# Optimization experiments

Hardware: AMD Instinct MI355X
Metric: run time of the kernel (lower is better)

The kernel has to match this reference:

```python
import jax, jax.numpy as jnp
import numpy as np

B, H, W, D = 16, 14, 14, 512   # map_dim D == attention_dim A (required by broadcast add)
L, HID, A = 32, 512, 512


def setup_inputs() -> dict:
    key = jax.random.key(0)
    ks = jax.random.split(key, 8)
    s = 0.02
    return {
        "maps": jax.random.normal(ks[0], (B, H, W, D), jnp.float32),
        "hiddens": jax.random.normal(ks[1], (B, L, HID), jnp.float32),
        "W_hidden": jax.random.normal(ks[2], (A, HID), jnp.float32) * s,
        "b_hidden": jnp.zeros((A,), jnp.float32),
        "W_rect": jax.random.normal(ks[3], (1, A), jnp.float32) * s,
        "b_rect": jnp.zeros((1,), jnp.float32),
        "W_co": jax.random.normal(ks[4], (HID, D), jnp.float32) * s,
        "b_co": jnp.zeros((HID,), jnp.float32),
    }


def reference(maps, hiddens, W_hidden, b_hidden, W_rect, b_rect, W_co, b_co):
    b, h, w, d = maps.shape
    fmaps = maps.reshape(b, h * w, d)                       # (B, P, D)
    hlin = hiddens @ W_hidden.T + b_hidden                  # (B, L, A)
    # additive co-attention score: ReLU(fmaps + hlin) -> linear to scalar
    rect = jax.nn.relu(fmaps[:, None, :, :] + hlin[:, :, None, :])  # (B, L, P, A)
    scores = jnp.einsum('blpa,a->blp', rect, W_rect[0]) + b_rect[0]  # (B, L, P)
    attn = jax.nn.softmax(scores, axis=2)                   # softmax over pixels P
    ctx = jnp.einsum('blp,bpd->bld', attn, fmaps)           # (B, L, D)
    co_att = (ctx @ W_co.T + b_co) * hiddens                # (B, L, HID)
    return co_att, attn
```

## Files before the change

### kernel.cpp

```cpp
#include <hip/hip_runtime.h>
#include <math.h>

#define Bn   16
#define Ln   32
#define Pn   196
#define BLn  512

typedef __attribute__((ext_vector_type(8))) short short8;
typedef __attribute__((ext_vector_type(4))) float f32x4;

__device__ __forceinline__ unsigned f2bf_u(float x) {
    union { float f; unsigned u; } c; c.f = x;
    return (c.u + 0x7FFFu + ((c.u >> 16) & 1u)) >> 16;
}
__device__ __forceinline__ unsigned short f2bf(float x) { return (unsigned short)f2bf_u(x); }
__device__ __forceinline__ unsigned pack2(float lo, float hi) {
    return f2bf_u(lo) | (f2bf_u(hi) << 16);
}
__device__ __forceinline__ uint4 pack8(const float4 a, const float4 b) {
    uint4 r;
    r.x = pack2(a.x, a.y); r.y = pack2(a.z, a.w);
    r.z = pack2(b.x, b.y); r.w = pack2(b.z, b.w);
    return r;
}

template<int MODE>
__global__ __launch_bounds__(64) void mfma_gemm(
    const float* __restrict__ Af, const unsigned short* __restrict__ Ab,
    const float* __restrict__ B, const float* __restrict__ bias,
    const float* __restrict__ hmul, float* __restrict__ C)
{
    const int m0 = blockIdx.x * 32, n0 = blockIdx.y * 32;
    const int lane = threadIdx.x;
    __shared__ uint4 As[2048];
    __shared__ uint4 Bs[2048];

    const int quad = lane >> 4, mp = lane & 15;
    #pragma unroll 4
    for (int i = 0; i < 32; ++i) {
        const int t = i & 1, s = i >> 1;
        const int row  = t * 16 + mp;
        const int col8 = s * 4 + quad;
        uint4 av;
        if (MODE == 0) {
            const float* ap = Af + (size_t)(m0 + row) * 512 + col8 * 8;
            av = pack8(*(const float4*)ap, *(const float4*)(ap + 4));
        } else {
            av = *(const uint4*)(Ab + (size_t)(m0 + row) * 512 + col8 * 8);
        }
        const float* bp = B + (size_t)(n0 + row) * 512 + col8 * 8;
        As[i * 64 + lane] = av;
        Bs[i * 64 + lane] = pack8(*(const float4*)bp, *(const float4*)(bp + 4));
    }
    __syncthreads();

    f32x4 acc00 = {0.f,0.f,0.f,0.f};
    f32x4 acc01 = acc00, acc10 = acc00, acc11 = acc00;
    #pragma unroll
    for (int s = 0; s < 16; ++s) {
        const short8 a0 = *reinterpret_cast<const short8*>(&As[(2*s+0)*64 + lane]);
        const short8 a1 = *reinterpret_cast<const short8*>(&As[(2*s+1)*64 + lane]);
        const short8 b0 = *reinterpret_cast<const short8*>(&Bs[(2*s+0)*64 + lane]);
        const short8 b1 = *reinterpret_cast<const short8*>(&Bs[(2*s+1)*64 + lane]);
        acc00 = __builtin_amdgcn_mfma_f32_16x16x32_bf16(a0, b0, acc00, 0, 0, 0);
        acc01 = __builtin_amdgcn_mfma_f32_16x16x32_bf16(a0, b1, acc01, 0, 0, 0);
        acc10 = __builtin_amdgcn_mfma_f32_16x16x32_bf16(a1, b0, acc10, 0, 0, 0);
        acc11 = __builtin_amdgcn_mfma_f32_16x16x32_bf16(a1, b1, acc11, 0, 0, 0);
    }

    const int row4 = quad * 4, col = mp;
    const f32x4 accs[2][2] = { {acc00, acc01}, {acc10, acc11} };
    #pragma unroll
    for (int tm = 0; tm < 2; ++tm)
        #pragma unroll
        for (int tn = 0; tn < 2; ++tn)
            #pragma unroll
            for (int r = 0; r < 4; ++r) {
                const int m = m0 + tm*16 + row4 + r, n = n0 + tn*16 + col;
                float v = accs[tm][tn][r] + bias[n];
                if (MODE == 1) v *= hmul[(size_t)m*512 + n];
                C[(size_t)m*512 + n] = v;
            }
}

__global__ __launch_bounds__(256) void scores_kernel(
    const float* __restrict__ maps, const float* __restrict__ hlin,
    const float* __restrict__ W_rect, const float* __restrict__ b_rect,
    float* __restrict__ scores_out)
{
    const int b = blockIdx.x, p0 = blockIdx.y * 14;
    const int tid = threadIdx.x;
    const int kc = tid >> 5, l = tid & 31;

    __shared__ float fls[14][516];
    __shared__ float hls[32][516];
    __shared__ float wls[516];
    __shared__ float red[4][14][32];

    const float* fbase = maps + ((size_t)b * Pn + p0) * 512;
    #pragma unroll
    for (int i = 0; i < 7; ++i) {
        const int fidx = i * 256 + tid;
        const int e = fidx * 4, p = e >> 9, c = e & 511;
        *(float4*)&fls[p][c] = *(const float4*)(fbase + (size_t)p * 512 + c);
    }
    const float* hbase = hlin + (size_t)b * 32 * 512;
    #pragma unroll
    for (int i = 0; i < 16; ++i) {
        const int fidx = i * 256 + tid;
        const int e = fidx * 4, r = e >> 9, c = e & 511;
        *(float4*)&hls[r][c] = *(const float4*)(hbase + (size_t)r * 512 + c);
    }
    if (tid < 128)
        *(float4*)&wls[tid * 4] = *(const float4*)(W_rect + tid * 4);
    __syncthreads();

    float acc[14];
    #pragma unroll
    for (int p = 0; p < 14; ++p) acc[p] = 0.f;

    const int off = kc * 64;
    for (int j4 = 0; j4 < 16; ++j4) {
        const float4 w4 = *(const float4*)&wls[off + j4 * 4];
        const float4 h4 = *(const float4*)&hls[l][off + j4 * 4];
        #pragma unroll
        for (int p = 0; p < 14; ++p) {
            const float4 f4 = *(const float4*)&fls[p][off + j4 * 4];
            acc[p] += fmaxf(f4.x + h4.x, 0.f) * w4.x + fmaxf(f4.y + h4.y, 0.f) * w4.y
                    + fmaxf(f4.z + h4.z, 0.f) * w4.z + fmaxf(f4.w + h4.w, 0.f) * w4.w;
        }
    }

    #pragma unroll
    for (int p = 0; p < 14; ++p) acc[p] += __shfl_down(acc[p], 32);
    const int wave = tid >> 6;
    if ((tid & 63) < 32) {
        #pragma unroll
        for (int p = 0; p < 14; ++p) red[wave][p][l] = acc[p];
    }
    __syncthreads();

    const float br = b_rect[0];
    const int l2 = tid & 31, pb = tid >> 5;
    for (int pp = pb; pp < 14; pp += 8) {
        const float s = red[0][pp][l2] + red[1][pp][l2] + red[2][pp][l2] + red[3][pp][l2] + br;
        scores_out[((size_t)b * 32 + l2) * Pn + p0 + pp] = s;
    }
}

__global__ __launch_bounds__(256) void softmax_ctx_kernel(
    const float* __restrict__ maps, const float* __restrict__ scores,
    float* __restrict__ attn_out, unsigned short* __restrict__ ctx_out)
{
    const int b = blockIdx.x, d0 = blockIdx.y * 32;
    const int tid = threadIdx.x;
    __shared__ float ft[196][36];
    __shared__ float at[32][204];

    const float* fbase = maps + (size_t)b * Pn * 512 + d0;
    for (int fidx = tid; fidx < 1568; fidx += 256) {
        const int p = fidx >> 3, q = fidx & 7;
        *(float4*)&ft[p][q * 4] = *(const float4*)(fbase + (size_t)p * 512 + q * 4);
    }
    const float4* sbase4 = (const float4*)(scores + (size_t)b * 32 * Pn);
    for (int fidx = tid; fidx < 1568; fidx += 256) {
        const int r = fidx / 49, c4 = fidx - r * 49;
        *(float4*)&at[r][c4 * 4] = sbase4[fidx];
    }
    __syncthreads();

    const int wave = tid >> 6, lane = tid & 63;
    #pragma unroll
    for (int rr = 0; rr < 8; ++rr) {
        const int row = wave * 8 + rr;
        float v[4];
        #pragma unroll
        for (int i = 0; i < 4; ++i) {
            const int p = lane + 64 * i;
            v[i] = (p < Pn) ? at[row][p] : -INFINITY;
        }
        float m = fmaxf(fmaxf(v[0], v[1]), fmaxf(v[2], v[3]));
        for (int off = 32; off > 0; off >>= 1) m = fmaxf(m, __shfl_down(m, off));
        m = __shfl(m, 0);
        float e[4], s = 0.f;
        #pragma unroll
        for (int i = 0; i < 4; ++i) {
            const int p = lane + 64 * i;
            e[i] = (p < Pn) ? __expf(v[i] - m) : 0.f;
            s += e[i];
        }
        for (int off = 32; off > 0; off >>= 1) s += __shfl_down(s, off);
        s = __shfl(s, 0);
        const float inv = 1.f / s;
        #pragma unroll
        for (int i = 0; i < 4; ++i) {
            const int p = lane + 64 * i;
            if (p < Pn) at[row][p] = e[i] * inv;
        }
    }
    __syncthreads();

    if (blockIdx.y == 0) {
        float4* ao4 = (float4*)(attn_out + (size_t)b * 32 * Pn);
        for (int fidx = tid; fidx < 1568; fidx += 256) {
            const int r = fidx / 49, c4 = fidx - r * 49;
            ao4[fidx] = *(const float4*)&at[r][c4 * 4];
        }
    }

    const int l = tid >> 3, d4 = tid & 7;
    float ax = 0.f, ay = 0.f, az = 0.f, aw = 0.f;
    for (int p4 = 0; p4 < 49; ++p4) {
        const float4 a4 = *(const float4*)&at[l][p4 * 4];
        const float4 f0 = *(const float4*)&ft[p4 * 4 + 0][d4 * 4];
        const float4 f1 = *(const float4*)&ft[p4 * 4 + 1][d4 * 4];
        const float4 f2 = *(const float4*)&ft[p4 * 4 + 2][d4 * 4];
        const float4 f3 = *(const float4*)&ft[p4 * 4 + 3][d4 * 4];
        ax += a4.x * f0.x + a4.y * f1.x + a4.z * f2.x + a4.w * f3.x;
        ay += a4.x * f0.y + a4.y * f1.y + a4.z * f2.y + a4.w * f3.y;
        az += a4.x * f0.z + a4.y * f1.z + a4.z * f2.z + a4.w * f3.z;
        aw += a4.x * f0.w + a4.y * f1.w + a4.z * f2.w + a4.w * f3.w;
    }
    ushort4 o;
    o.x = f2bf(ax); o.y = f2bf(ay); o.z = f2bf(az); o.w = f2bf(aw);
    *(ushort4*)(ctx_out + ((size_t)b * 32 + l) * 512 + d0 + d4 * 4) = o;
}

extern "C" void kernel_launch(void* const* d_in, const int* in_sizes, int n_in,
                              void* d_out, int out_size, void* d_ws, size_t ws_size,
                              hipStream_t stream)
{
    const float* maps     = (const float*)d_in[0];
    const float* hiddens  = (const float*)d_in[1];
    const float* W_hidden = (const float*)d_in[2];
    const float* b_hidden = (const float*)d_in[3];
    const float* W_rect   = (const float*)d_in[4];
    const float* b_rect   = (const float*)d_in[5];
    const float* W_co     = (const float*)d_in[6];
    const float* b_co     = (const float*)d_in[7];

    float* out_co   = (float*)d_out;
    float* out_attn = out_co + (size_t)BLn * 512;

    char* ws = (char*)d_ws;
    float*          scores = (float*)(ws);
    unsigned short* ctx16  = (unsigned short*)(ws + (512 << 10));

    hipLaunchKernelGGL((mfma_gemm<0>), dim3(16, 16), dim3(64), 0, stream,
                       hiddens, (const unsigned short*)nullptr, W_hidden, b_hidden,
                       (const float*)nullptr, out_co);
    hipLaunchKernelGGL(scores_kernel, dim3(Bn, 14), dim3(256), 0, stream,
                       maps, out_co, W_rect, b_rect, scores);
    hipLaunchKernelGGL(softmax_ctx_kernel, dim3(Bn, 16), dim3(256), 0, stream,
                       maps, scores, out_attn, ctx16);
    hipLaunchKernelGGL((mfma_gemm<1>), dim3(16, 16), dim3(64), 0, stream,
                       (const float*)nullptr, ctx16, W_co, b_co, hiddens, out_co);
}
```

Baseline: 111.5 us.

## Fuse four kernels into one persistent kernel with software grid barriers

Replaces the four separate launches (hidden GEMM, scores, softmax+ctx, output GEMM) with one persistent kernel of 224 blocks that runs the phases in turn, separated by atomic-counter grid barriers reset by a memset. It also reworks the GEMM tiles to split K across 4 waves with an LDS reduction, and changes the scores phase to keep each pixel's feature slice in registers while looping over the 32 hidden rows. The aim is to remove inter-kernel launch gaps. In exchange it relies on all 224 blocks being co-resident for the spin barriers, and some phases leave blocks idle or serialize tiles.

```diff
diff --git a/kernel.cpp b/kernel.cpp
--- a/kernel.cpp
+++ b/kernel.cpp
@@ -1,10 +1,7 @@
 #include <hip/hip_runtime.h>
 #include <math.h>
 
-#define Bn   16
-#define Ln   32
-#define Pn   196
-#define BLn  512
+#define NBLK 224
 
 typedef __attribute__((ext_vector_type(8))) short short8;
 typedef __attribute__((ext_vector_type(4))) float f32x4;
@@ -24,206 +21,250 @@
     return r;
 }
 
+__device__ __forceinline__ void gridbar(int* bar, int idx) {
+    __syncthreads();
+    if (threadIdx.x == 0) {
+        __hip_atomic_fetch_add(&bar[idx], 1, __ATOMIC_ACQ_REL, __HIP_MEMORY_SCOPE_AGENT);
+        while (__hip_atomic_load(&bar[idx], __ATOMIC_ACQUIRE, __HIP_MEMORY_SCOPE_AGENT) < NBLK) {
+            __builtin_amdgcn_s_sleep(2);
+        }
+    }
+    __syncthreads();
+}
+
 template<int MODE>
-__global__ __launch_bounds__(64) void mfma_gemm(
+__device__ __forceinline__ void gemm_phase(
     const float* __restrict__ Af, const unsigned short* __restrict__ Ab,
-    const float* __restrict__ B, const float* __restrict__ bias,
-    const float* __restrict__ hmul, float* __restrict__ C)
-{
-    const int m0 = blockIdx.x * 32, n0 = blockIdx.y * 32;
-    const int lane = threadIdx.x;
-    __shared__ uint4 As[2048];
-    __shared__ uint4 Bs[2048];
-
-    const int quad = lane >> 4, mp = lane & 15;
-    #pragma unroll 4
-    for (int i = 0; i < 32; ++i) {
-        const int t = i & 1, s = i >> 1;
-        const int row  = t * 16 + mp;
-        const int col8 = s * 4 + quad;
-        uint4 av;
-        if (MODE == 0) {
-            const float* ap = Af + (size_t)(m0 + row) * 512 + col8 * 8;
-            av = pack8(*(const float4*)ap, *(const float4*)(ap + 4));
-        } else {
-            av = *(const uint4*)(Ab + (size_t)(m0 + row) * 512 + col8 * 8);
-        }
-        const float* bp = B + (size_t)(n0 + row) * 512 + col8 * 8;
-        As[i * 64 + lane] = av;
-        Bs[i * 64 + lane] = pack8(*(const float4*)bp, *(const float4*)(bp + 4));
-    }
-    __syncthreads();
-
-    f32x4 acc00 = {0.f,0.f,0.f,0.f};
-    f32x4 acc01 = acc00, acc10 = acc00, acc11 = acc00;
-    #pragma unroll
-    for (int s = 0; s < 16; ++s) {
-        const short8 a0 = *reinterpret_cast<const short8*>(&As[(2*s+0)*64 + lane]);
-        const short8 a1 = *reinterpret_cast<const short8*>(&As[(2*s+1)*64 + lane]);
-        const short8 b0 = *reinterpret_cast<const short8*>(&Bs[(2*s+0)*64 + lane]);
-        const short8 b1 = *reinterpret_cast<const short8*>(&Bs[(2*s+1)*64 + lane]);
-        acc00 = __builtin_amdgcn_mfma_f32_16x16x32_bf16(a0, b0, acc00, 0, 0, 0);
-        acc01 = __builtin_amdgcn_mfma_f32_16x16x32_bf16(a0, b1, acc01, 0, 0, 0);
-        acc10 = __builtin_amdgcn_mfma_f32_16x16x32_bf16(a1, b0, acc10, 0, 0, 0);
-        acc11 = __builtin_amdgcn_mfma_f32_16x16x32_bf16(a1, b1, acc11, 0, 0, 0);
-    }
-
-    const int row4 = quad * 4, col = mp;
-    const f32x4 accs[2][2] = { {acc00, acc01}, {acc10, acc11} };
-    #pragma unroll
-    for (int tm = 0; tm < 2; ++tm)
-        #pragma unroll
-        for (int tn = 0; tn < 2; ++tn)
-            #pragma unroll
-            for (int r = 0; r < 4; ++r) {
-                const int m = m0 + tm*16 + row4 + r, n = n0 + tn*16 + col;
-                float v = accs[tm][tn][r] + bias[n];
-                if (MODE == 1) v *= hmul[(size_t)m*512 + n];
-                C[(size_t)m*512 + n] = v;
-            }
-}
-
-__global__ __launch_bounds__(256) void scores_kernel(
+    const float* __restrict__ Bf, const float* __restrict__ bias,
+    const float* __restrict__ hmul, float* __restrict__ C, char* smem, int bid)
+{
+    uint4* As = (uint4*)smem;
+    uint4* Bs = (uint4*)(smem + 32768);
+    float* red = (float*)smem;
+    const int tid = threadIdx.x;
+
+    for (int tile = bid; tile < 256; tile += NBLK) {
+        const int m0 = (tile >> 4) * 32, n0 = (tile & 15) * 32;
+        __syncthreads();
+        #pragma unroll
+        for (int j = 0; j < 8; ++j) {
+            const int S = tid + 256 * j;
+            const int i = S >> 6, ln = S & 63;
+            const int t = i & 1, s = i >> 1;
+            const int row  = t * 16 + (ln & 15);
+            const int col8 = s * 4 + (ln >> 4);
+            uint4 av;
+            if (MODE == 0) {
+                const float* ap = Af + (size_t)(m0 + row) * 512 + col8 * 8;
+                av = pack8(*(const float4*)ap, *(const float4*)(ap + 4));
+            } else {
+                av = *(const uint4*)(Ab + (size_t)(m0 + row) * 512 + col8 * 8);
+            }
+            const float* bp = Bf + (size_t)(n0 + row) * 512 + col8 * 8;
+            As[S] = av;
+            Bs[S] = pack8(*(const float4*)bp, *(const float4*)(bp + 4));
+        }
+        __syncthreads();
+
+        const int w = tid >> 6, ln = tid & 63;
+        f32x4 acc[4];
+        #pragma unroll
+        for (int fo = 0; fo < 4; ++fo) acc[fo] = (f32x4){0.f,0.f,0.f,0.f};
+        #pragma unroll
+        for (int sl = 0; sl < 4; ++sl) {
+            const int s = 4 * w + sl;
+            const short8 a0 = *(const short8*)&As[(2*s+0)*64 + ln];
+            const short8 a1 = *(const short8*)&As[(2*s+1)*64 + ln];
+            const short8 b0 = *(const short8*)&Bs[(2*s+0)*64 + ln];
+            const short8 b1 = *(const short8*)&Bs[(2*s+1)*64 + ln];
+            acc[0] = __builtin_amdgcn_mfma_f32_16x16x32_bf16(a0, b0, acc[0], 0, 0, 0);
+            acc[1] = __builtin_amdgcn_mfma_f32_16x16x32_bf16(a0, b1, acc[1], 0, 0, 0);
+            acc[2] = __builtin_amdgcn_mfma_f32_16x16x32_bf16(a1, b0, acc[2], 0, 0, 0);
+            acc[3] = __builtin_amdgcn_mfma_f32_16x16x32_bf16(a1, b1, acc[3], 0, 0, 0);
+        }
+        __syncthreads();
+        #pragma unroll
+        for (int fo = 0; fo < 4; ++fo)
+            #pragma unroll
+            for (int r = 0; r < 4; ++r)
+                red[w*1024 + fo*256 + r*64 + ln] = acc[fo][r];
+        __syncthreads();
+        #pragma unroll
+        for (int j = 0; j < 4; ++j) {
+            const int o = tid + 256 * j;
+            float v = red[o] + red[1024 + o] + red[2048 + o] + red[3072 + o];
+            const int fo = o >> 8, r = (o >> 6) & 3, l2 = o & 63;
+            const int m = m0 + (fo >> 1) * 16 + ((l2 >> 4) << 2) + r;
+            const int n = n0 + (fo & 1) * 16 + (l2 & 15);
+            v += bias[n];
+            if (MODE == 1) v *= hmul[(size_t)m * 512 + n];
+            C[(size_t)m * 512 + n] = v;
+        }
+    }
+}
+
+__device__ __forceinline__ void scores_phase(
     const float* __restrict__ maps, const float* __restrict__ hlin,
     const float* __restrict__ W_rect, const float* __restrict__ b_rect,
-    float* __restrict__ scores_out)
-{
-    const int b = blockIdx.x, p0 = blockIdx.y * 14;
+    float* __restrict__ scores_out, char* smem, int bid)
+{
+    float* hls  = (float*)smem;
+    float* redb = (float*)smem;
     const int tid = threadIdx.x;
-    const int kc = tid >> 5, l = tid & 31;
-
-    __shared__ float fls[14][516];
-    __shared__ float hls[32][516];
-    __shared__ float wls[516];
-    __shared__ float red[4][14][32];
-
-    const float* fbase = maps + ((size_t)b * Pn + p0) * 512;
+    const int b = bid / 14, p0 = (bid % 14) * 14;
+    const int kc = tid >> 4, pslot = tid & 15;
+    const int p = p0 + (pslot < 14 ? pslot : 13);
+
+    __syncthreads();
+    const float4* hg = (const float4*)(hlin + (size_t)b * 32 * 512);
+    float4* h4 = (float4*)hls;
     #pragma unroll
-    for (int i = 0; i < 7; ++i) {
-        const int fidx = i * 256 + tid;
-        const int e = fidx * 4, p = e >> 9, c = e & 511;
-        *(float4*)&fls[p][c] = *(const float4*)(fbase + (size_t)p * 512 + c);
-    }
-    const float* hbase = hlin + (size_t)b * 32 * 512;
+    for (int j = 0; j < 16; ++j) h4[tid + 256 * j] = hg[tid + 256 * j];
+
+    float4 fr[8], wr[8];
+    const float* fb = maps + ((size_t)b * 196 + p) * 512 + kc * 32;
+    const float* wb = W_rect + kc * 32;
     #pragma unroll
-    for (int i = 0; i < 16; ++i) {
-        const int fidx = i * 256 + tid;
-        const int e = fidx * 4, r = e >> 9, c = e & 511;
-        *(float4*)&hls[r][c] = *(const float4*)(hbase + (size_t)r * 512 + c);
-    }
-    if (tid < 128)
-        *(float4*)&wls[tid * 4] = *(const float4*)(W_rect + tid * 4);
-    __syncthreads();
-
-    float acc[14];
-    #pragma unroll
-    for (int p = 0; p < 14; ++p) acc[p] = 0.f;
-
-    const int off = kc * 64;
-    for (int j4 = 0; j4 < 16; ++j4) {
-        const float4 w4 = *(const float4*)&wls[off + j4 * 4];
-        const float4 h4 = *(const float4*)&hls[l][off + j4 * 4];
-        #pragma unroll
-        for (int p = 0; p < 14; ++p) {
-            const float4 f4 = *(const float4*)&fls[p][off + j4 * 4];
-            acc[p] += fmaxf(f4.x + h4.x, 0.f) * w4.x + fmaxf(f4.y + h4.y, 0.f) * w4.y
-                    + fmaxf(f4.z + h4.z, 0.f) * w4.z + fmaxf(f4.w + h4.w, 0.f) * w4.w;
-        }
-    }
-
-    #pragma unroll
-    for (int p = 0; p < 14; ++p) acc[p] += __shfl_down(acc[p], 32);
-    const int wave = tid >> 6;
-    if ((tid & 63) < 32) {
-        #pragma unroll
-        for (int p = 0; p < 14; ++p) red[wave][p][l] = acc[p];
-    }
-    __syncthreads();
-
+    for (int j = 0; j < 8; ++j) {
+        fr[j] = *(const float4*)(fb + 4 * j);
+        wr[j] = *(const float4*)(wb + 4 * j);
+    }
+    __syncthreads();
+
+    float acc[32];
+    for (int l = 0; l < 32; ++l) {
+        const float* hrow = hls + l * 512 + kc * 32;
+        float s0 = 0.f, s1 = 0.f, s2 = 0.f, s3 = 0.f;
+        #pragma unroll
+        for (int j = 0; j < 8; ++j) {
+            const float4 h = *(const float4*)(hrow + 4 * j);
+            const float4 f = fr[j], w = wr[j];
+            s0 += fmaxf(f.x + h.x, 0.f) * w.x;
+            s1 += fmaxf(f.y + h.y, 0.f) * w.y;
+            s2 += fmaxf(f.z + h.z, 0.f) * w.z;
+            s3 += fmaxf(f.w + h.w, 0.f) * w.w;
+        }
+        acc[l] = (s0 + s1) + (s2 + s3);
+    }
+    __syncthreads();
+    #pragma unroll 4
+    for (int l = 0; l < 32; ++l)
+        redb[pslot * 545 + l * 17 + kc] = acc[l];
+    __syncthreads();
     const float br = b_rect[0];
-    const int l2 = tid & 31, pb = tid >> 5;
-    for (int pp = pb; pp < 14; pp += 8) {
-        const float s = red[0][pp][l2] + red[1][pp][l2] + red[2][pp][l2] + red[3][pp][l2] + br;
-        scores_out[((size_t)b * 32 + l2) * Pn + p0 + pp] = s;
-    }
-}
-
-__global__ __launch_bounds__(256) void softmax_ctx_kernel(
+    for (int q = tid; q < 448; q += 256) {
+        const int pp = q >> 5, l = q & 31;
+        const float* rb = redb + pp * 545 + l * 17;
+        float s = 0.f;
+        #pragma unroll
+        for (int k = 0; k < 16; ++k) s += rb[k];
+        scores_out[((size_t)b * 32 + l) * 196 + p0 + pp] = s + br;
+    }
+}
+
+__device__ __forceinline__ void softmax_ctx_phase(
     const float* __restrict__ maps, const float* __restrict__ scores,
-    float* __restrict__ attn_out, unsigned short* __restrict__ ctx_out)
-{
-    const int b = blockIdx.x, d0 = blockIdx.y * 32;
+    float* __restrict__ attn_out, unsigned short* __restrict__ ctx_out,
+    char* smem, int bid)
+{
+    float* ft = (float*)smem;
+    float* at = (float*)(smem + 28224);
     const int tid = threadIdx.x;
-    __shared__ float ft[196][36];
-    __shared__ float at[32][204];
-
-    const float* fbase = maps + (size_t)b * Pn * 512 + d0;
-    for (int fidx = tid; fidx < 1568; fidx += 256) {
-        const int p = fidx >> 3, q = fidx & 7;
-        *(float4*)&ft[p][q * 4] = *(const float4*)(fbase + (size_t)p * 512 + q * 4);
-    }
-    const float4* sbase4 = (const float4*)(scores + (size_t)b * 32 * Pn);
-    for (int fidx = tid; fidx < 1568; fidx += 256) {
-        const int r = fidx / 49, c4 = fidx - r * 49;
-        *(float4*)&at[r][c4 * 4] = sbase4[fidx];
-    }
-    __syncthreads();
-
-    const int wave = tid >> 6, lane = tid & 63;
-    #pragma unroll
-    for (int rr = 0; rr < 8; ++rr) {
-        const int row = wave * 8 + rr;
-        float v[4];
-        #pragma unroll
-        for (int i = 0; i < 4; ++i) {
-            const int p = lane + 64 * i;
-            v[i] = (p < Pn) ? at[row][p] : -INFINITY;
-        }
-        float m = fmaxf(fmaxf(v[0], v[1]), fmaxf(v[2], v[3]));
-        for (int off = 32; off > 0; off >>= 1) m = fmaxf(m, __shfl_down(m, off));
-        m = __shfl(m, 0);
-        float e[4], s = 0.f;
-        #pragma unroll
-        for (int i = 0; i < 4; ++i) {
-            const int p = lane + 64 * i;
-            e[i] = (p < Pn) ? __expf(v[i] - m) : 0.f;
-            s += e[i];
-        }
-        for (int off = 32; off > 0; off >>= 1) s += __shfl_down(s, off);
-        s = __shfl(s, 0);
-        const float inv = 1.f / s;
-        #pragma unroll
-        for (int i = 0; i < 4; ++i) {
-            const int p = lane + 64 * i;
-            if (p < Pn) at[row][p] = e[i] * inv;
-        }
-    }
-    __syncthreads();
-
-    if (blockIdx.y == 0) {
-        float4* ao4 = (float4*)(attn_out + (size_t)b * 32 * Pn);
+
+    for (int tile = bid; tile < 256; tile += NBLK) {
+        const int b = tile >> 4, d0 = (tile & 15) * 32;
+        __syncthreads();
+        const float* fbase = maps + (size_t)b * 196 * 512 + d0;
+        for (int fidx = tid; fidx < 1568; fidx += 256) {
+            const int pp = fidx >> 3, q = fidx & 7;
+            *(float4*)&ft[pp * 36 + q * 4] = *(const float4*)(fbase + (size_t)pp * 512 + q * 4);
+        }
+        const float4* sbase4 = (const float4*)(scores + (size_t)b * 32 * 196);
         for (int fidx = tid; fidx < 1568; fidx += 256) {
             const int r = fidx / 49, c4 = fidx - r * 49;
-            ao4[fidx] = *(const float4*)&at[r][c4 * 4];
-        }
-    }
-
-    const int l = tid >> 3, d4 = tid & 7;
-    float ax = 0.f, ay = 0.f, az = 0.f, aw = 0.f;
-    for (int p4 = 0; p4 < 49; ++p4) {
-        const float4 a4 = *(const float4*)&at[l][p4 * 4];
-        const float4 f0 = *(const float4*)&ft[p4 * 4 + 0][d4 * 4];
-        const float4 f1 = *(const float4*)&ft[p4 * 4 + 1][d4 * 4];
-        const float4 f2 = *(const float4*)&ft[p4 * 4 + 2][d4 * 4];
-        const float4 f3 = *(const float4*)&ft[p4 * 4 + 3][d4 * 4];
-        ax += a4.x * f0.x + a4.y * f1.x + a4.z * f2.x + a4.w * f3.x;
-        ay += a4.x * f0.y + a4.y * f1.y + a4.z * f2.y + a4.w * f3.y;
-        az += a4.x * f0.z + a4.y * f1.z + a4.z * f2.z + a4.w * f3.z;
-        aw += a4.x * f0.w + a4.y * f1.w + a4.z * f2.w + a4.w * f3.w;
-    }
-    ushort4 o;
-    o.x = f2bf(ax); o.y = f2bf(ay); o.z = f2bf(az); o.w = f2bf(aw);
-    *(ushort4*)(ctx_out + ((size_t)b * 32 + l) * 512 + d0 + d4 * 4) = o;
+            *(float4*)&at[r * 204 + c4 * 4] = sbase4[fidx];
+        }
+        __syncthreads();
+
+        const int wave = tid >> 6, lane = tid & 63;
+        #pragma unroll
+        for (int rr = 0; rr < 8; ++rr) {
+            const int row = wave * 8 + rr;
+            float v[4];
+            #pragma unroll
+            for (int i = 0; i < 4; ++i) {
+                const int pp = lane + 64 * i;
+                v[i] = (pp < 196) ? at[row * 204 + pp] : -INFINITY;
+            }
+            float m = fmaxf(fmaxf(v[0], v[1]), fmaxf(v[2], v[3]));
+            for (int off = 32; off > 0; off >>= 1) m = fmaxf(m, __shfl_down(m, off));
+            m = __shfl(m, 0);
+            float e[4], s = 0.f;
+            #pragma unroll
+            for (int i = 0; i < 4; ++i) {
+                const int pp = lane + 64 * i;
+                e[i] = (pp < 196) ? __expf(v[i] - m) : 0.f;
+                s += e[i];
+            }
+            for (int off = 32; off > 0; off >>= 1) s += __shfl_down(s, off);
+            s = __shfl(s, 0);
+            const float inv = 1.f / s;
+            #pragma unroll
+            for (int i = 0; i < 4; ++i) {
+                const int pp = lane + 64 * i;
+                if (pp < 196) at[row * 204 + pp] = e[i] * inv;
+            }
+        }
+        __syncthreads();
+
+        if ((tile & 15) == 0) {
+            float4* ao4 = (float4*)(attn_out + (size_t)b * 32 * 196);
+            for (int fidx = tid; fidx < 1568; fidx += 256) {
+                const int r = fidx / 49, c4 = fidx - r * 49;
+                ao4[fidx] = *(const float4*)&at[r * 204 + c4 * 4];
+            }
+        }
+
+        const int l = tid >> 3, d4 = tid & 7;
+        float ax = 0.f, ay = 0.f, az = 0.f, aw = 0.f;
+        for (int p4 = 0; p4 < 49; ++p4) {
+            const float4 a4 = *(const float4*)&at[l * 204 + p4 * 4];
+            const float4 f0 = *(const float4*)&ft[(p4 * 4 + 0) * 36 + d4 * 4];
+            const float4 f1 = *(const float4*)&ft[(p4 * 4 + 1) * 36 + d4 * 4];
+            const float4 f2 = *(const float4*)&ft[(p4 * 4 + 2) * 36 + d4 * 4];
+            const float4 f3 = *(const float4*)&ft[(p4 * 4 + 3) * 36 + d4 * 4];
+            ax += a4.x * f0.x + a4.y * f1.x + a4.z * f2.x + a4.w * f3.x;
+            ay += a4.x * f0.y + a4.y * f1.y + a4.z * f2.y + a4.w * f3.y;
+            az += a4.x * f0.z + a4.y * f1.z + a4.z * f2.z + a4.w * f3.z;
+            aw += a4.x * f0.w + a4.y * f1.w + a4.z * f2.w + a4.w * f3.w;
+        }
+        ushort4 o;
+        o.x = f2bf(ax); o.y = f2bf(ay); o.z = f2bf(az); o.w = f2bf(aw);
+        *(ushort4*)(ctx_out + ((size_t)b * 32 + l) * 512 + d0 + d4 * 4) = o;
+        __syncthreads();
+    }
+}
+
+__global__ __launch_bounds__(256) void coatt_mega_kernel(
+    const float* __restrict__ maps, const float* __restrict__ hiddens,
+    const float* __restrict__ W_hidden, const float* __restrict__ b_hidden,
+    const float* __restrict__ W_rect, const float* __restrict__ b_rect,
+    const float* __restrict__ W_co, const float* __restrict__ b_co,
+    float* __restrict__ out_co, float* __restrict__ out_attn,
+    float* __restrict__ scores, unsigned short* __restrict__ ctx16,
+    int* __restrict__ bar)
+{
+    __shared__ __align__(16) char smem[65536];
+    const int bid = blockIdx.x;
+
+    gemm_phase<0>(hiddens, (const unsigned short*)nullptr, W_hidden, b_hidden,
+                  (const float*)nullptr, out_co, smem, bid);
+    gridbar(bar, 0);
+    scores_phase(maps, out_co, W_rect, b_rect, scores, smem, bid);
+    gridbar(bar, 1);
+    softmax_ctx_phase(maps, scores, out_attn, ctx16, smem, bid);
+    gridbar(bar, 2);
+    gemm_phase<1>((const float*)nullptr, ctx16, W_co, b_co, hiddens, out_co, smem, bid);
 }
 
 extern "C" void kernel_launch(void* const* d_in, const int* in_sizes, int n_in,
@@ -240,19 +281,15 @@
     const float* b_co     = (const float*)d_in[7];
 
     float* out_co   = (float*)d_out;
-    float* out_attn = out_co + (size_t)BLn * 512;
+    float* out_attn = out_co + (size_t)512 * 512;
 
     char* ws = (char*)d_ws;
     float*          scores = (float*)(ws);
-    unsigned short* ctx16  = (unsigned short*)(ws + (512 << 10));
-
-    hipLaunchKernelGGL((mfma_gemm<0>), dim3(16, 16), dim3(64), 0, stream,
-                       hiddens, (const unsigned short*)nullptr, W_hidden, b_hidden,
-                       (const float*)nullptr, out_co);
-    hipLaunchKernelGGL(scores_kernel, dim3(Bn, 14), dim3(256), 0, stream,
-                       maps, out_co, W_rect, b_rect, scores);
-    hipLaunchKernelGGL(softmax_ctx_kernel, dim3(Bn, 16), dim3(256), 0, stream,
-                       maps, scores, out_attn, ctx16);
-    hipLaunchKernelGGL((mfma_gemm<1>), dim3(16, 16), dim3(64), 0, stream,
-                       (const float*)nullptr, ctx16, W_co, b_co, hiddens, out_co);
-}
+    unsigned short* ctx16  = (unsigned short*)(ws + (1 << 20));
+    int*            bar    = (int*)(ws + (4 << 20));
+
+    hipMemsetAsync(bar, 0, 64, stream);
+    hipLaunchKernelGGL(coatt_mega_kernel, dim3(NBLK), dim3(256), 0, stream,
+                       maps, hiddens, W_hidden, b_hidden, W_rect, b_rect,
+                       W_co, b_co, out_co, out_attn, scores, ctx16, bar);
+}
```

Result: slower. 182.5 us (+63.8%).
